# Performance work log

Hardware: AMD Instinct MI355X
Metric: run time of the kernel (lower is better)

The kernel has to match this reference:

```python
import jax, jax.numpy as jnp
import numpy as np

EPS = 1.0  # global `epsilon` in the original code
B, C, N, T = 4, 32, 256, 288
NUM_PRED, NUM_LOCAL = 12, 12
PERIOD, SHORT, LONG = 24, 12, 48
EMB = 16
RE_K = 5  # ResidualExtrapolate kernel width (num_input)


def const_extrap(x, p):
    # replicate-pad right by p along time
    return jnp.concatenate([x, jnp.repeat(x[..., -1:], p, axis=-1)], axis=-1)


def seasonal_extrap(x, p):
    # circular-pad right by p along time (p <= t)
    return jnp.concatenate([x, x[..., :p]], axis=-1)


def term_norm(x, L):
    # sliding-window mean/var over last axis, window L, replicate-padded left.
    pad1 = [(0, 0)] * 3 + [(1, 0)]
    cs = jnp.pad(jnp.cumsum(x, axis=-1), pad1)
    cs2 = jnp.pad(jnp.cumsum(x * x, axis=-1), pad1)
    mean = (cs[..., L:] - cs[..., :-L]) / L            # (b,c,n,t-L+1)
    var = (cs2[..., L:] - cs2[..., :-L]) / L - mean ** 2 + 1e-5
    padL = [(0, 0)] * 3 + [(L - 1, 0)]
    mean = jnp.pad(mean, padL, mode='edge')
    var = jnp.pad(var, padL, mode='edge')
    out = (x - mean) / jnp.sqrt(var + EPS)
    return out, mean, jnp.sqrt(var)


def seasonal_norm(x, P):
    b, c, n, t = x.shape
    xp = x.reshape(b, c, n, t // P, P)
    mean = xp.mean(3)                                   # (b,c,n,P) per-phase
    var = (xp ** 2).mean(3) - mean ** 2 + 1e-5
    mean = jnp.tile(mean, (1, 1, 1, t // P))
    var = jnp.tile(var, (1, 1, 1, t // P))
    out = (x - mean) / jnp.sqrt(var + EPS)
    return out, mean, jnp.sqrt(var)


def spatial_norm(x, emb):
    n = emb.shape[0]
    adj = emb @ emb.T - 10.0 * jnp.eye(n, dtype=x.dtype)
    adj = jax.nn.softmax(adj, axis=-1)                  # (n,n)
    mean = jnp.einsum('nm,bcmt->bcnt', adj, x)
    var = jnp.einsum('nm,bcmt->bcnt', adj, x * x) - mean ** 2 + 1e-5
    out = (x - mean) / jnp.sqrt(var + EPS)
    return out, mean, jnp.sqrt(var)


def residual_extrap(x, W, bias):
    # Conv2d(c -> c*num_pred, kernel (1, RE_K)) on last RE_K steps, then cat.
    b, c, n, t = x.shape
    y = jnp.einsum('ock,bcnk->bon', W[:, :, 0, :], x[..., -RE_K:]) + bias[None, :, None]
    proj = y.reshape(b, NUM_PRED, c, n).transpose(0, 2, 3, 1)  # (b,c,n,num_pred)
    return jnp.concatenate([x, proj], axis=-1)


def conv_time(x, W, bias):
    y = jax.lax.conv_general_dilated(x, W, (1, 1), 'VALID',
                                     dimension_numbers=('NCHW', 'OIHW', 'NCHW'))
    return y + bias[None, :, None, None]


def conv1x1(x, W, bias):
    return jnp.einsum('oc,bcnt->bont', W[:, :, 0, 0], x) + bias[None, :, None, None]


def setup_inputs() -> dict:
    key = jax.random.key(0)
    ks = jax.random.split(key, 16)
    f32 = jnp.float32

    def w(k, shape, fan_in):
        return jax.random.normal(k, shape, dtype=f32) / np.sqrt(fan_in)

    inp = {
        'x': jax.random.normal(ks[0], (B, C, N, T), dtype=f32),
        'node_embedding': 0.1 * jax.random.normal(ks[1], (N, EMB), dtype=f32),
        'conv1_w': w(ks[6], (C, 13 * C, 1, NUM_LOCAL), 13 * C * NUM_LOCAL),
        'conv1_b': jnp.zeros((C,), f32),
        'conv2_w': w(ks[7], (C, 13 * C, 1, NUM_LOCAL), 13 * C * NUM_LOCAL),
        'conv2_b': jnp.zeros((C,), f32),
        'skip_w': w(ks[8], (C, C, 1, 1), C),
        'skip_b': jnp.zeros((C,), f32),
        'res_w': w(ks[9], (C, C, 1, 1), C),
        'res_b': jnp.zeros((C,), f32),
    }
    for i in range(4):
        inp[f're{i + 1}_w'] = w(ks[2 + i], (C * NUM_PRED, C, 1, RE_K), C * RE_K)
        inp[f're{i + 1}_b'] = jnp.zeros((C * NUM_PRED,), f32)
    return inp


def reference(x, node_embedding, conv1_w, conv1_b, conv2_w, conv2_b,
              skip_w, skip_b, res_w, res_b,
              re1_w, re1_b, re2_w, re2_b, re3_w, re3_b, re4_w, re4_b):
    xs, aux = [], []

    x_proj = const_extrap(x, NUM_PRED)
    zeros = jnp.zeros_like(x_proj)
    xs.append(x_proj); aux.append(zeros)

    x1, lt_mean, lt_std = term_norm(x, LONG)
    xp = residual_extrap(x1, re1_w, re1_b)
    mp, sp = const_extrap(lt_mean, NUM_PRED), const_extrap(lt_std, NUM_PRED)
    xs += [xp, mp, sp]; aux += [zeros, mp, sp]

    x2, se_mean, se_std = seasonal_norm(x1, PERIOD)
    xp = residual_extrap(x2, re2_w, re2_b)
    mp, sp = seasonal_extrap(se_mean, NUM_PRED), seasonal_extrap(se_std, NUM_PRED)
    xs += [xp, mp, sp]; aux += [zeros, mp, sp]

    x3, st_mean, st_std = term_norm(x2, SHORT)
    xp = residual_extrap(x3, re3_w, re3_b)
    mp, sp = const_extrap(st_mean, NUM_PRED), const_extrap(st_std, NUM_PRED)
    xs += [xp, mp, sp]; aux += [zeros, mp, sp]

    x4, sn_mean, sn_std = spatial_norm(x3, node_embedding)
    xp = residual_extrap(x4, re4_w, re4_b)
    mp, sp = const_extrap(sn_mean, NUM_PRED), const_extrap(sn_std, NUM_PRED)
    xs += [xp, mp, sp]; aux += [zeros, mp, sp]

    pad1 = [(0, 0)] * 3 + [(1, 0)]
    x_cat = jnp.pad(jnp.concatenate(xs, axis=1), pad1)      # (b,13c,n,T+P+1)
    a_cat = jnp.pad(jnp.concatenate(aux, axis=1), pad1)

    g1 = conv_time(x_cat, conv1_w, conv1_b)
    g2 = conv_time(x_cat, conv2_w, conv2_b)
    a1 = conv_time(a_cat, conv1_w, conv1_b)
    a2 = conv_time(a_cat, conv2_w, conv2_b)

    prod = g1 * g2
    x_z = conv1x1(prod[..., :-NUM_PRED], res_w, res_b)
    s = conv1x1(prod[..., -NUM_PRED:], skip_w, skip_b)
    s_aux = conv1x1((a1 * a2)[..., -NUM_PRED:], skip_w, skip_b)
    return (x_z, s_aux, s)
```

## Files before the change

### kernel.cpp

```cpp
#include <hip/hip_runtime.h>

typedef unsigned short u16;
typedef __attribute__((ext_vector_type(8))) short short8v;
typedef __attribute__((ext_vector_type(4))) float f32x4;

#define PSTR 304L
#define OFF_SAUX 9109504L
#define OFF_S    9502720L
#define CHSTR (32L*256L*PSTR)

static __device__ __forceinline__ float bf2f(u16 u) {
  return __uint_as_float(((unsigned int)u) << 16);
}
static __device__ __forceinline__ u16 f2bf(float f) {
  unsigned int i = __float_as_uint(f);
  i += 0x7FFFu + ((i >> 16) & 1u);
  return (u16)(i >> 16);
}

static __device__ __forceinline__ void gload16(const void* g, void* l) {
  __builtin_amdgcn_global_load_lds(
      (const __attribute__((address_space(1))) unsigned int*)g,
      (__attribute__((address_space(3))) unsigned int*)l, 16, 0, 0);
}

static __device__ void adj_body(int row, const float* __restrict__ emb,
                                u16* __restrict__ adjb) {
  const int m = threadIdx.x;
  __shared__ float sred[8];
  float er[16];
#pragma unroll
  for (int e = 0; e < 16; ++e) er[e] = emb[row * 16 + e];
  float d = 0.f;
#pragma unroll
  for (int e = 0; e < 16; ++e) d += er[e] * emb[m * 16 + e];
  if (m == row) d -= 10.f;
  float v = d;
#pragma unroll
  for (int off = 32; off; off >>= 1) v = fmaxf(v, __shfl_xor(v, off, 64));
  const int wid = m >> 6, lane = m & 63;
  if (lane == 0) sred[wid] = v;
  __syncthreads();
  const float mx = fmaxf(fmaxf(sred[0], sred[1]), fmaxf(sred[2], sred[3]));
  const float p = expf(d - mx);
  v = p;
#pragma unroll
  for (int off = 32; off; off >>= 1) v += __shfl_xor(v, off, 64);
  if (lane == 0) sred[4 + wid] = v;
  __syncthreads();
  const float sum = sred[4] + sred[5] + sred[6] + sred[7];
  adjb[row * 256 + m] = f2bf(p / sum);
}

static __device__ void prepw_body(int bid, const float* __restrict__ c1w,
                                  const float* __restrict__ c2w,
                                  u16* __restrict__ wB) {
  const int idx = bid * 256 + threadIdx.x;
  const int kk = idx >> 11;
  const int rem = idx & 2047;
  const int j = rem >> 5, chp = rem & 31;
  const int pslot = chp >> 3, chlo = chp & 7;
  const int sl = pslot ^ ((j >> 1) & 3);
  const int ch = sl * 8 + chlo;
  const int g = kk / 12, k = kk - g * 12;
  const int cin = g * 32 + ch;
  const float* src = (j < 32) ? c1w : c2w;
  const int jj = j & 31;
  wB[idx] = f2bf(src[(jj * 416 + cin) * 12 + k]);
}

static __device__ __forceinline__ void wscan2(float& s1, float& s2, int lane) {
#pragma unroll
  for (int off = 1; off < 64; off <<= 1) {
    float a = __shfl_up(s1, off, 64);
    float b = __shfl_up(s2, off, 64);
    if (lane >= off) { s1 += a; s2 += b; }
  }
}

static __device__ void norm_body(int bid, const float* __restrict__ x,
                                 u16* __restrict__ xcat) {
  const int wid = threadIdx.x >> 6, lane = threadIdx.x & 63;
  const long row = (long)bid * 4 + wid;
  const int b = (int)(row >> 13);
  const int c = (int)((row >> 8) & 31);
  const int n = (int)(row & 255);
  const float* xr = x + row * 288;
  __shared__ float bufA[4][304], bufB[4][304], cs1[4][312], cs2[4][312], sst[4][80];
  float* bA = bufA[wid];
  float* bB = bufB[wid];
  float* p1 = cs1[wid];
  float* p2 = cs2[wid];
  float* psm = sst[wid];
  float* psi = sst[wid] + 24;
  float* psd = sst[wid] + 48;
  const long chb = (long)b * 416 * 256 + n;

  for (int j = 0; j < 5; ++j) { int t = j * 64 + lane; if (t < 288) bA[t] = xr[t]; }

  auto scanbuf = [&](float* src) {
    float ca = 0.f, cb = 0.f;
    if (lane == 0) { p1[0] = 0.f; p2[0] = 0.f; }
    for (int j = 0; j < 5; ++j) {
      int t = j * 64 + lane;
      float v = (t < 288) ? src[t] : 0.f;
      float s1 = v, s2 = v * v;
      wscan2(s1, s2, lane);
      if (t < 288) { p1[t + 1] = ca + s1; p2[t + 1] = cb + s2; }
      ca += __shfl(s1, 63, 64);
      cb += __shfl(s2, 63, 64);
    }
  };

  scanbuf(bA);
  for (int j = 0; j < 5; ++j) {
    int t = j * 64 + lane; if (t >= 288) continue;
    float S, Q;
    if (t >= 47) { S = p1[t + 1] - p1[t - 47]; Q = p2[t + 1] - p2[t - 47]; }
    else         { S = p1[48];                 Q = p2[48]; }
    float m = S * (1.f / 48.f);
    float var = Q * (1.f / 48.f) - m * m + 1e-5f;
    float sd = sqrtf(var);
    float iv = rsqrtf(var + 1.f);
    float xv = bA[t];
    float x1 = (xv - m) * iv;
    bB[t] = x1;
    xcat[(chb + (long)(c)      * 256) * PSTR + 1 + t] = f2bf(xv);
    xcat[(chb + (long)(32 + c) * 256) * PSTR + 1 + t] = f2bf(x1);
    xcat[(chb + (long)(64 + c) * 256) * PSTR + 1 + t] = f2bf(m);
    xcat[(chb + (long)(96 + c) * 256) * PSTR + 1 + t] = f2bf(sd);
  }
  {
    float S = p1[288] - p1[240], Q = p2[288] - p2[240];
    float m = S * (1.f / 48.f);
    float var = Q * (1.f / 48.f) - m * m + 1e-5f;
    float sd = sqrtf(var);
    if (lane < 12) {
      xcat[(chb + (long)(c)      * 256) * PSTR + 289 + lane] = f2bf(bA[287]);
      xcat[(chb + (long)(64 + c) * 256) * PSTR + 289 + lane] = f2bf(m);
      xcat[(chb + (long)(96 + c) * 256) * PSTR + 289 + lane] = f2bf(sd);
    }
    if (lane == 0) {
      xcat[(chb + (long)(c)      * 256) * PSTR] = 0;
      xcat[(chb + (long)(32 + c) * 256) * PSTR] = 0;
      xcat[(chb + (long)(64 + c) * 256) * PSTR] = 0;
      xcat[(chb + (long)(96 + c) * 256) * PSTR] = 0;
    }
  }
  if (lane < 24) {
    float S = 0.f, Q = 0.f;
#pragma unroll
    for (int i2 = 0; i2 < 12; ++i2) { float v = bB[lane + 24 * i2]; S += v; Q += v * v; }
    float m = S * (1.f / 12.f);
    float var = Q * (1.f / 12.f) - m * m + 1e-5f;
    psm[lane] = m; psi[lane] = rsqrtf(var + 1.f); psd[lane] = sqrtf(var);
  }
  for (int j = 0; j < 5; ++j) {
    int t = j * 64 + lane; if (t >= 288) continue;
    int ph = t % 24;
    float m = psm[ph];
    float x2v = (bB[t] - m) * psi[ph];
    bA[t] = x2v;
    xcat[(chb + (long)(128 + c) * 256) * PSTR + 1 + t] = f2bf(x2v);
    xcat[(chb + (long)(160 + c) * 256) * PSTR + 1 + t] = f2bf(m);
    xcat[(chb + (long)(192 + c) * 256) * PSTR + 1 + t] = f2bf(psd[ph]);
  }
  if (lane < 12) {
    xcat[(chb + (long)(160 + c) * 256) * PSTR + 289 + lane] = f2bf(psm[lane]);
    xcat[(chb + (long)(192 + c) * 256) * PSTR + 289 + lane] = f2bf(psd[lane]);
  }
  if (lane == 0) {
    xcat[(chb + (long)(128 + c) * 256) * PSTR] = 0;
    xcat[(chb + (long)(160 + c) * 256) * PSTR] = 0;
    xcat[(chb + (long)(192 + c) * 256) * PSTR] = 0;
  }
  scanbuf(bA);
  for (int j = 0; j < 5; ++j) {
    int t = j * 64 + lane; if (t >= 288) continue;
    float S, Q;
    if (t >= 11) { S = p1[t + 1] - p1[t - 11]; Q = p2[t + 1] - p2[t - 11]; }
    else         { S = p1[12];                 Q = p2[12]; }
    float m = S * (1.f / 12.f);
    float var = Q * (1.f / 12.f) - m * m + 1e-5f;
    float sd = sqrtf(var);
    float iv = rsqrtf(var + 1.f);
    float x3v = (bA[t] - m) * iv;
    xcat[(chb + (long)(224 + c) * 256) * PSTR + 1 + t] = f2bf(x3v);
    xcat[(chb + (long)(256 + c) * 256) * PSTR + 1 + t] = f2bf(m);
    xcat[(chb + (long)(288 + c) * 256) * PSTR + 1 + t] = f2bf(sd);
  }
  {
    float S = p1[288] - p1[276], Q = p2[288] - p2[276];
    float m = S * (1.f / 12.f);
    float var = Q * (1.f / 12.f) - m * m + 1e-5f;
    float sd = sqrtf(var);
    if (lane < 12) {
      xcat[(chb + (long)(256 + c) * 256) * PSTR + 289 + lane] = f2bf(m);
      xcat[(chb + (long)(288 + c) * 256) * PSTR + 289 + lane] = f2bf(sd);
    }
    if (lane == 0) {
      xcat[(chb + (long)(224 + c) * 256) * PSTR] = 0;
      xcat[(chb + (long)(256 + c) * 256) * PSTR] = 0;
      xcat[(chb + (long)(288 + c) * 256) * PSTR] = 0;
    }
  }
}

__global__ __launch_bounds__(256) void k_front(const float* __restrict__ x,
    const float* __restrict__ emb, const float* __restrict__ c1w,
    const float* __restrict__ c2w, u16* __restrict__ xcat,
    u16* __restrict__ adjb, u16* __restrict__ wB) {
  const int bid = blockIdx.x;
  if (bid < 8192)       norm_body(bid, x, xcat);
  else if (bid < 8448)  adj_body(bid - 8192, emb, adjb);
  else                  prepw_body(bid - 8448, c1w, c2w, wB);
}

static __device__ void re_body(long gid, u16* __restrict__ xcat,
                               const float* __restrict__ W,
                               const float* __restrict__ bias, int srcch) {
  const int o = (int)(gid % 384);
  const long bn = gid / 384;
  const int n = (int)(bn & 255);
  const int b = (int)(bn >> 8);
  const float* wr = W + o * 160;
  float acc = bias[o];
  for (int c = 0; c < 32; ++c) {
    const long rb = ((long)(b * 416 + srcch + c) * 256 + n) * PSTR + 284;
#pragma unroll
    for (int k = 0; k < 5; ++k) acc += wr[c * 5 + k] * bf2f(xcat[rb + k]);
  }
  const int cd = o & 31, p = o >> 5;
  xcat[((long)(b * 416 + srcch + cd) * 256 + n) * PSTR + 289 + p] = f2bf(acc);
}

__global__ __launch_bounds__(256) void k_re4(u16* __restrict__ xcat,
                                             const float* __restrict__ W,
                                             const float* __restrict__ bias) {
  re_body((long)blockIdx.x * 256 + threadIdx.x, xcat, W, bias, 320);
}

static __device__ void spatial_body(int sid, u16* __restrict__ xcat,
                                    const u16* __restrict__ adjb) {
  const int gx = sid % 20;
  const int slice = sid / 20;
  const int tcn = gx >> 2, ncb = gx & 3;
  const int b = slice >> 5, c = slice & 31;
  const int t0 = tcn * 64, n0 = ncb * 64;
  const int tid = threadIdx.x;
  const int wid = tid >> 6, lane = tid & 63;
  const int wm = wid >> 1, wn = wid & 1;
  const int l15 = lane & 15, lq = lane >> 4;
  __shared__ __align__(16) u16 BT[2][64 * 40];
  __shared__ __align__(16) u16 BT2[2][64 * 40];
  const f32x4 vz = {0.f, 0.f, 0.f, 0.f};
  f32x4 aM[2][2], aV[2][2];
#pragma unroll
  for (int i = 0; i < 2; ++i)
#pragma unroll
    for (int j = 0; j < 2; ++j) { aM[i][j] = vz; aV[i][j] = vz; }
  const long base7 = (long)(b * 416 + 224 + c) * 256;
  u16 rv[8];
#pragma unroll
  for (int r = 0; r < 8; ++r) {
    int idx = tid + r * 256; int ml = idx >> 6, s = idx & 63;
    rv[r] = xcat[(base7 + ml) * PSTR + 1 + t0 + s];
  }
#pragma unroll
  for (int r = 0; r < 8; ++r) {
    int idx = tid + r * 256; int ml = idx >> 6, s = idx & 63;
    float v = bf2f(rv[r]);
    BT[0][s * 40 + ml] = rv[r];
    BT2[0][s * 40 + ml] = f2bf(v * v);
  }
  __syncthreads();
  int cur = 0;
  for (int kk = 0; kk < 8; ++kk) {
    u16 rn[8];
    if (kk < 7) {
#pragma unroll
      for (int r = 0; r < 8; ++r) {
        int idx = tid + r * 256; int ml = idx >> 6, s = idx & 63;
        rn[r] = xcat[(base7 + (long)((kk + 1) * 32 + ml)) * PSTR + 1 + t0 + s];
      }
    }
    const short8v a0 = *(const short8v*)(adjb + (long)(n0 + wm * 32 + l15) * 256 + kk * 32 + lq * 8);
    const short8v a1 = *(const short8v*)(adjb + (long)(n0 + wm * 32 + 16 + l15) * 256 + kk * 32 + lq * 8);
    const u16* bt = BT[cur];
    const u16* bq = BT2[cur];
    const short8v b0 = *(const short8v*)(bt + (wn * 32 + l15) * 40 + lq * 8);
    const short8v b1 = *(const short8v*)(bt + (wn * 32 + 16 + l15) * 40 + lq * 8);
    const short8v q0 = *(const short8v*)(bq + (wn * 32 + l15) * 40 + lq * 8);
    const short8v q1 = *(const short8v*)(bq + (wn * 32 + 16 + l15) * 40 + lq * 8);
    aM[0][0] = __builtin_amdgcn_mfma_f32_16x16x32_bf16(a0, b0, aM[0][0], 0, 0, 0);
    aM[0][1] = __builtin_amdgcn_mfma_f32_16x16x32_bf16(a0, b1, aM[0][1], 0, 0, 0);
    aM[1][0] = __builtin_amdgcn_mfma_f32_16x16x32_bf16(a1, b0, aM[1][0], 0, 0, 0);
    aM[1][1] = __builtin_amdgcn_mfma_f32_16x16x32_bf16(a1, b1, aM[1][1], 0, 0, 0);
    aV[0][0] = __builtin_amdgcn_mfma_f32_16x16x32_bf16(a0, q0, aV[0][0], 0, 0, 0);
    aV[0][1] = __builtin_amdgcn_mfma_f32_16x16x32_bf16(a0, q1, aV[0][1], 0, 0, 0);
    aV[1][0] = __builtin_amdgcn_mfma_f32_16x16x32_bf16(a1, q0, aV[1][0], 0, 0, 0);
    aV[1][1] = __builtin_amdgcn_mfma_f32_16x16x32_bf16(a1, q1, aV[1][1], 0, 0, 0);
    __syncthreads();
    if (kk < 7) {
#pragma unroll
      for (int r = 0; r < 8; ++r) {
        int idx = tid + r * 256; int ml = idx >> 6, s = idx & 63;
        float v = bf2f(rn[r]);
        BT[cur ^ 1][s * 40 + ml] = rn[r];
        BT2[cur ^ 1][s * 40 + ml] = f2bf(v * v);
      }
    }
    __syncthreads();
    cur ^= 1;
  }
#pragma unroll
  for (int mf = 0; mf < 2; ++mf)
#pragma unroll
    for (int nf = 0; nf < 2; ++nf)
#pragma unroll
      for (int e = 0; e < 4; ++e) {
        const int i = wm * 32 + mf * 16 + lq * 4 + e;
        const int j = wn * 32 + nf * 16 + l15;
        const int nn = n0 + i, tt2 = t0 + j;
        if (tt2 < 288) {
          const float mean = aM[mf][nf][e], ex2 = aV[mf][nf][e];
          const float var = ex2 - mean * mean + 1e-5f;
          const float sd = sqrtf(var);
          const float iv = rsqrtf(var + 1.f);
          const float x3c = bf2f(xcat[(base7 + nn) * PSTR + 1 + tt2]);
          const float x4 = (x3c - mean) * iv;
          const long r10 = ((long)(b * 416 + 320 + c) * 256 + nn) * PSTR;
          const long r11 = ((long)(b * 416 + 352 + c) * 256 + nn) * PSTR;
          const long r12 = ((long)(b * 416 + 384 + c) * 256 + nn) * PSTR;
          xcat[r10 + 1 + tt2] = f2bf(x4);
          xcat[r11 + 1 + tt2] = f2bf(mean);
          xcat[r12 + 1 + tt2] = f2bf(sd);
          if (tt2 == 287) {
            for (int p = 0; p < 12; ++p) {
              xcat[r11 + 289 + p] = f2bf(mean);
              xcat[r12 + 289 + p] = f2bf(sd);
            }
          }
          if (tt2 == 0) { xcat[r10] = 0; xcat[r11] = 0; xcat[r12] = 0; }
        }
      }
}

__global__ __launch_bounds__(256) void k_mid(u16* __restrict__ xcat,
    const u16* __restrict__ adjb,
    const float* __restrict__ w1, const float* __restrict__ b1,
    const float* __restrict__ w2, const float* __restrict__ b2,
    const float* __restrict__ w3, const float* __restrict__ b3) {
  const int bid = blockIdx.x;
  if (bid < 2560) { spatial_body(bid, xcat, adjb); return; }
  const int sub = bid - 2560;
  const int which = sub / 1536;
  const long gid = (long)(sub - which * 1536) * 256 + threadIdx.x;
  if (which == 0)      re_body(gid, xcat, w1, b1, 32);
  else if (which == 1) re_body(gid, xcat, w2, b2, 128);
  else                 re_body(gid, xcat, w3, b3, 224);
}

__global__ __launch_bounds__(256, 3) void k_convG(
    const u16* __restrict__ xcat, const u16* __restrict__ wB,
    const float* __restrict__ c1b, const float* __restrict__ c2b,
    const float* __restrict__ rsw, const float* __restrict__ rsb,
    const float* __restrict__ skw, const float* __restrict__ skb,
    float* __restrict__ out) {
  const int tc = blockIdx.x;
  const int by = blockIdx.y;
  const int b = by >> 6;
  const int tid = threadIdx.x;
  const int wid = tid >> 6, lane = tid & 63;
  const int n_abs = (by & 63) * 4 + wid;
  const int t0 = tc * 64;
  const int l15 = lane & 15, lq = lane >> 4;

  __shared__ __align__(16) unsigned char smem[41984];
  u16* Asm = (u16*)smem;
  u16* Bsm = (u16*)(smem + 25600);

  int sch[5], stk[5];
  const u16* baseR[5];
#pragma unroll
  for (int r = 0; r < 5; ++r) {
    int cc = r * 64 + lane;
    int s = cc / 10;
    int tk = cc - s * 10;
    sch[r] = s; stk[r] = tk;
    baseR[r] = xcat + ((long)(b * 416 + s) * 256 + n_abs) * PSTR + t0 + tk * 8;
  }
  u16* aw = Asm + wid * 3200;

#define AWRITE() { \
    _Pragma("unroll") \
    for (int r = 0; r < 5; ++r) { \
      u16 pc[8]; *(uint4*)pc = aR[r]; \
      const int pcol = ((((sch[r] >> 3) ^ stk[r]) & 3) << 3) + (sch[r] & 7); \
      _Pragma("unroll") \
      for (int e = 0; e < 8; ++e) aw[(stk[r] * 8 + e) * 40 + pcol] = pc[e]; \
    } }

  uint4 aR[5];
#pragma unroll
  for (int r = 0; r < 5; ++r) aR[r] = *(const uint4*)baseR[r];
  AWRITE();
#pragma unroll
  for (int r = 0; r < 5; ++r) aR[r] = *(const uint4*)(baseR[r] + CHSTR);
  gload16(wB + 0 * 2048 + wid * 512 + lane * 8, Bsm + 0 + wid * 512);
  gload16(wB + 1 * 2048 + wid * 512 + lane * 8, Bsm + 2048 + wid * 512);
  __syncthreads();

  const f32x4 vz = {0.f, 0.f, 0.f, 0.f};
  f32x4 acc[4][4];
#pragma unroll
  for (int i = 0; i < 4; ++i)
#pragma unroll
    for (int j = 0; j < 4; ++j) acc[i][j] = vz;

  const u16* bwl = Bsm + l15 * 32 + ((lq ^ ((l15 >> 1) & 3)) << 3);

  int p = 0;
  for (int g = 0; g < 13; ++g) {
    for (int kp = 0; kp < 6; ++kp) {
      if (p < 77) {
        const long kkn = (long)(p + 1) * 2;
        const int bufn = ((p + 1) & 1) * 4096;
        gload16(wB + kkn * 2048 + wid * 512 + lane * 8, Bsm + bufn + wid * 512);
        gload16(wB + (kkn + 1) * 2048 + wid * 512 + lane * 8, Bsm + bufn + 2048 + wid * 512);
      }
      const int bufc = (p & 1) * 4096;
#pragma unroll
      for (int kh = 0; kh < 2; ++kh) {
        const int K = kp * 2 + kh;
        short8v af[4], bf[4];
#pragma unroll
        for (int f = 0; f < 4; ++f) {
          const int tt = K + f * 16 + l15;
          af[f] = *(const short8v*)(aw + tt * 40 + (((lq ^ (tt >> 3)) & 3) << 3));
        }
#pragma unroll
        for (int f = 0; f < 4; ++f)
          bf[f] = *(const short8v*)(bwl + bufc + kh * 2048 + f * 512);
#pragma unroll
        for (int i = 0; i < 4; ++i)
#pragma unroll
          for (int j = 0; j < 4; ++j)
            acc[i][j] = __builtin_amdgcn_mfma_f32_16x16x32_bf16(af[i], bf[j], acc[i][j], 0, 0, 0);
      }
      __syncthreads();
      ++p;
    }
    if (g < 12) {
      AWRITE();
      if (g < 11) {
#pragma unroll
        for (int r = 0; r < 5; ++r) aR[r] = *(const uint4*)(baseR[r] + (long)(g + 2) * CHSTR);
      }
    }
  }
#undef AWRITE
  __syncthreads();

  float* pw = (float*)smem + wid * 2112;
#pragma unroll
  for (int fi = 0; fi < 4; ++fi)
#pragma unroll
    for (int nf = 0; nf < 2; ++nf)
#pragma unroll
      for (int e = 0; e < 4; ++e) {
        const int trow = fi * 16 + lq * 4 + e;
        const int cch = nf * 16 + l15;
        const float g1 = acc[fi][nf][e] + c1b[cch];
        const float g2 = acc[fi][nf + 2][e] + c2b[cch];
        pw[trow * 33 + cch] = g1 * g2;
      }
  float pv[32];
  {
    const float* prow = pw + lane * 33;
#pragma unroll
    for (int c = 0; c < 32; ++c) pv[c] = prow[c];
  }
  const int t = t0 + lane;
  if (t0 + 63 < 278) {
    for (int o = 0; o < 32; ++o) {
      float s = rsb[o];
      const float* wr = rsw + o * 32;
#pragma unroll
      for (int c = 0; c < 32; ++c) s += wr[c] * pv[c];
      out[((long)(b * 32 + o) * 256 + n_abs) * 278 + t] = s;
    }
  } else {
    const bool isres = t < 278;
    const bool isskip = (t >= 278) && (t < 290);
    for (int o = 0; o < 32; ++o) {
      const float* wr = (isres ? rsw : skw) + o * 32;
      float s = (isres ? rsb : skb)[o];
#pragma unroll
      for (int c = 0; c < 32; ++c) s += wr[c] * pv[c];
      if (isres)       out[((long)(b * 32 + o) * 256 + n_abs) * 278 + t] = s;
      else if (isskip) out[OFF_S + ((long)(b * 32 + o) * 256 + n_abs) * 12 + (t - 278)] = s;
    }
  }
}

__global__ __launch_bounds__(256) void k_convA(const u16* __restrict__ xcat,
    const u16* __restrict__ wB, const float* __restrict__ c1b,
    const float* __restrict__ c2b, const float* __restrict__ skw,
    const float* __restrict__ skb, float* __restrict__ out) {
  const int tid = threadIdx.x;
  const int wid = tid >> 6, lane = tid & 63;
  const int row = blockIdx.x;
  const int b = row >> 8, n = row & 255;
  const int l15 = lane & 15, lq = lane >> 4;
  __shared__ __align__(16) u16 ATa[4][2][36 * 40];
  __shared__ float apL[4][16 * 68];
  const int gtab[8] = {2, 3, 5, 6, 8, 9, 11, 12};
  const long bnbase = (long)b * 416 * 256 + n;

#pragma unroll
  for (int tau = 0; tau < 2; ++tau) {
    const int g = gtab[wid * 2 + tau];
    u16* at = ATa[wid][tau];
#pragma unroll
    for (int h = 0; h < 2; ++h) {
      const int c = lane + h * 64;
      const int ch = c >> 2, part = c & 3;
      const uint4 v = *(const uint4*)(xcat +
          (bnbase + (long)(g * 32 + ch) * 256) * PSTR + 272 + part * 8);
      u16 pc[8]; *(uint4*)pc = v;
#pragma unroll
      for (int e = 0; e < 8; ++e) at[(part * 8 + e) * 40 + ch] = pc[e];
    }
  }

  const f32x4 vz = {0.f, 0.f, 0.f, 0.f};
  f32x4 acc[4] = {vz, vz, vz, vz};
  const int bsw = (lq ^ ((l15 >> 1) & 3)) << 3;
#pragma unroll
  for (int tau = 0; tau < 2; ++tau) {
    const int g = gtab[wid * 2 + tau];
    const u16* at = ATa[wid][tau];
    for (int k = 0; k < 12; ++k) {
      const short8v af = *(const short8v*)(at + (l15 + k + 6) * 40 + lq * 8);
#pragma unroll
      for (int nf = 0; nf < 4; ++nf) {
        const short8v bf = *(const short8v*)(wB + (long)(g * 12 + k) * 2048 + (nf * 16 + l15) * 32 + bsw);
        acc[nf] = __builtin_amdgcn_mfma_f32_16x16x32_bf16(af, bf, acc[nf], 0, 0, 0);
      }
    }
  }
  float* ap = apL[wid];
#pragma unroll
  for (int nf = 0; nf < 4; ++nf)
#pragma unroll
    for (int e = 0; e < 4; ++e)
      ap[(lq * 4 + e) * 68 + nf * 16 + l15] = acc[nf][e];
  __syncthreads();
  for (int idx = tid; idx < 1024; idx += 256) {
    const int m = idx >> 6, j = idx & 63;
    apL[0][m * 68 + j] = apL[0][m * 68 + j] + apL[1][m * 68 + j]
                       + apL[2][m * 68 + j] + apL[3][m * 68 + j];
  }
  __syncthreads();
  for (int task = tid; task < 384; task += 256) {
    const int o = task & 31, tt = task >> 5;
    float s = skb[o];
#pragma unroll
    for (int c2 = 0; c2 < 32; ++c2)
      s += skw[o * 32 + c2] * (apL[0][tt * 68 + c2] + c1b[c2])
                            * (apL[0][tt * 68 + 32 + c2] + c2b[c2]);
    out[OFF_SAUX + ((long)(b * 32 + o) * 256 + n) * 12 + tt] = s;
  }
}

extern "C" void kernel_launch(void* const* d_in, const int* in_sizes, int n_in,
                              void* d_out, int out_size, void* d_ws, size_t ws_size,
                              hipStream_t stream) {
  const float* x   = (const float*)d_in[0];
  const float* emb = (const float*)d_in[1];
  const float* c1w = (const float*)d_in[2];
  const float* c1b = (const float*)d_in[3];
  const float* c2w = (const float*)d_in[4];
  const float* c2b = (const float*)d_in[5];
  const float* skw = (const float*)d_in[6];
  const float* skb = (const float*)d_in[7];
  const float* rsw = (const float*)d_in[8];
  const float* rsb = (const float*)d_in[9];
  float* out = (float*)d_out;

  u16* xcat = (u16*)d_ws;
  u16* wB   = xcat + (4L * 416 * 256 * 304 + 2048);
  u16* adjb = wB + 156L * 2048;

  k_front<<<dim3(9696), dim3(256), 0, stream>>>(x, emb, c1w, c2w, xcat, adjb, wB);
  k_mid<<<dim3(7168), dim3(256), 0, stream>>>(xcat, adjb,
      (const float*)d_in[10], (const float*)d_in[11],
      (const float*)d_in[12], (const float*)d_in[13],
      (const float*)d_in[14], (const float*)d_in[15]);
  k_re4<<<dim3(1536), dim3(256), 0, stream>>>(xcat, (const float*)d_in[16], (const float*)d_in[17]);
  k_convG<<<dim3(5, 256), dim3(256), 0, stream>>>(xcat, wB, c1b, c2b, rsw, rsb, skw, skb, out);
  k_convA<<<dim3(1024), dim3(256), 0, stream>>>(xcat, wB, c1b, c2b, skw, skb, out);
}
```

Measured before the change: 676.7 us.

## Widen convG time tile to 128 so each weight tile feeds more MFMAs

The gated conv kernel now has a templated body. The first two time-chunks of each row handle 128 time steps per block (8 M-fragments), and the last chunk keeps 64, so the grid drops from 5 to 3 blocks in x. The goal is to reuse every B (weight) tile loaded into LDS over twice as many MFMAs and to cut the count of redundant weight streams. In exchange the kernel uses more accumulator registers and more LDS (62 KB), occupancy falls to 2 blocks per CU, and the blocks are unevenly loaded.

```diff
diff --git a/kernel.cpp b/kernel.cpp
--- a/kernel.cpp
+++ b/kernel.cpp
@@ -361,60 +361,58 @@
   else                 re_body(gid, xcat, w3, b3, 224);
 }
 
-__global__ __launch_bounds__(256, 3) void k_convG(
+template<int MT>
+static __device__ void convG_body(int t0, int by,
     const u16* __restrict__ xcat, const u16* __restrict__ wB,
     const float* __restrict__ c1b, const float* __restrict__ c2b,
     const float* __restrict__ rsw, const float* __restrict__ rsb,
     const float* __restrict__ skw, const float* __restrict__ skb,
-    float* __restrict__ out) {
-  const int tc = blockIdx.x;
-  const int by = blockIdx.y;
+    float* __restrict__ out, unsigned char* smem) {
   const int b = by >> 6;
   const int tid = threadIdx.x;
   const int wid = tid >> 6, lane = tid & 63;
   const int n_abs = (by & 63) * 4 + wid;
-  const int t0 = tc * 64;
   const int l15 = lane & 15, lq = lane >> 4;
-
-  __shared__ __align__(16) unsigned char smem[41984];
+  constexpr int NCH = (MT == 2) ? 9 : 5;
+  constexpr int TKS = (MT == 2) ? 18 : 10;
+
   u16* Asm = (u16*)smem;
-  u16* Bsm = (u16*)(smem + 25600);
-
-  int sch[5], stk[5];
-  const u16* baseR[5];
-#pragma unroll
-  for (int r = 0; r < 5; ++r) {
+  u16* Bsm = (u16*)(smem + 46080);
+
+  int sch[NCH], stk[NCH];
+  const u16* baseR[NCH];
+#pragma unroll
+  for (int r = 0; r < NCH; ++r) {
     int cc = r * 64 + lane;
-    int s = cc / 10;
-    int tk = cc - s * 10;
+    int s = cc / TKS, tk = cc - s * TKS;
     sch[r] = s; stk[r] = tk;
     baseR[r] = xcat + ((long)(b * 416 + s) * 256 + n_abs) * PSTR + t0 + tk * 8;
   }
-  u16* aw = Asm + wid * 3200;
+  u16* aw = Asm + wid * 5760;
 
 #define AWRITE() { \
     _Pragma("unroll") \
-    for (int r = 0; r < 5; ++r) { \
+    for (int r = 0; r < NCH; ++r) { \
       u16 pc[8]; *(uint4*)pc = aR[r]; \
       const int pcol = ((((sch[r] >> 3) ^ stk[r]) & 3) << 3) + (sch[r] & 7); \
       _Pragma("unroll") \
       for (int e = 0; e < 8; ++e) aw[(stk[r] * 8 + e) * 40 + pcol] = pc[e]; \
     } }
 
-  uint4 aR[5];
-#pragma unroll
-  for (int r = 0; r < 5; ++r) aR[r] = *(const uint4*)baseR[r];
+  uint4 aR[NCH];
+#pragma unroll
+  for (int r = 0; r < NCH; ++r) aR[r] = *(const uint4*)baseR[r];
   AWRITE();
 #pragma unroll
-  for (int r = 0; r < 5; ++r) aR[r] = *(const uint4*)(baseR[r] + CHSTR);
+  for (int r = 0; r < NCH; ++r) aR[r] = *(const uint4*)(baseR[r] + CHSTR);
   gload16(wB + 0 * 2048 + wid * 512 + lane * 8, Bsm + 0 + wid * 512);
   gload16(wB + 1 * 2048 + wid * 512 + lane * 8, Bsm + 2048 + wid * 512);
   __syncthreads();
 
   const f32x4 vz = {0.f, 0.f, 0.f, 0.f};
-  f32x4 acc[4][4];
-#pragma unroll
-  for (int i = 0; i < 4; ++i)
+  f32x4 acc[4 * MT][4];
+#pragma unroll
+  for (int i = 0; i < 4 * MT; ++i)
 #pragma unroll
     for (int j = 0; j < 4; ++j) acc[i][j] = vz;
 
@@ -433,9 +431,9 @@
 #pragma unroll
       for (int kh = 0; kh < 2; ++kh) {
         const int K = kp * 2 + kh;
-        short8v af[4], bf[4];
-#pragma unroll
-        for (int f = 0; f < 4; ++f) {
+        short8v af[4 * MT], bf[4];
+#pragma unroll
+        for (int f = 0; f < 4 * MT; ++f) {
           const int tt = K + f * 16 + l15;
           af[f] = *(const short8v*)(aw + tt * 40 + (((lq ^ (tt >> 3)) & 3) << 3));
         }
@@ -443,7 +441,7 @@
         for (int f = 0; f < 4; ++f)
           bf[f] = *(const short8v*)(bwl + bufc + kh * 2048 + f * 512);
 #pragma unroll
-        for (int i = 0; i < 4; ++i)
+        for (int i = 0; i < 4 * MT; ++i)
 #pragma unroll
           for (int j = 0; j < 4; ++j)
             acc[i][j] = __builtin_amdgcn_mfma_f32_16x16x32_bf16(af[i], bf[j], acc[i][j], 0, 0, 0);
@@ -455,53 +453,69 @@
       AWRITE();
       if (g < 11) {
 #pragma unroll
-        for (int r = 0; r < 5; ++r) aR[r] = *(const uint4*)(baseR[r] + (long)(g + 2) * CHSTR);
+        for (int r = 0; r < NCH; ++r) aR[r] = *(const uint4*)(baseR[r] + (long)(g + 2) * CHSTR);
       }
     }
   }
 #undef AWRITE
   __syncthreads();
 
-  float* pw = (float*)smem + wid * 2112;
-#pragma unroll
-  for (int fi = 0; fi < 4; ++fi)
-#pragma unroll
-    for (int nf = 0; nf < 2; ++nf)
-#pragma unroll
-      for (int e = 0; e < 4; ++e) {
-        const int trow = fi * 16 + lq * 4 + e;
-        const int cch = nf * 16 + l15;
-        const float g1 = acc[fi][nf][e] + c1b[cch];
-        const float g2 = acc[fi][nf + 2][e] + c2b[cch];
-        pw[trow * 33 + cch] = g1 * g2;
-      }
-  float pv[32];
-  {
-    const float* prow = pw + lane * 33;
-#pragma unroll
-    for (int c = 0; c < 32; ++c) pv[c] = prow[c];
-  }
-  const int t = t0 + lane;
-  if (t0 + 63 < 278) {
-    for (int o = 0; o < 32; ++o) {
-      float s = rsb[o];
-      const float* wr = rsw + o * 32;
-#pragma unroll
-      for (int c = 0; c < 32; ++c) s += wr[c] * pv[c];
-      out[((long)(b * 32 + o) * 256 + n_abs) * 278 + t] = s;
-    }
-  } else {
-    const bool isres = t < 278;
-    const bool isskip = (t >= 278) && (t < 290);
-    for (int o = 0; o < 32; ++o) {
-      const float* wr = (isres ? rsw : skw) + o * 32;
-      float s = (isres ? rsb : skb)[o];
-#pragma unroll
-      for (int c = 0; c < 32; ++c) s += wr[c] * pv[c];
-      if (isres)       out[((long)(b * 32 + o) * 256 + n_abs) * 278 + t] = s;
-      else if (isskip) out[OFF_S + ((long)(b * 32 + o) * 256 + n_abs) * 12 + (t - 278)] = s;
-    }
-  }
+#pragma unroll
+  for (int pass = 0; pass < MT; ++pass) {
+    float* pw = (float*)smem + wid * 2112;
+#pragma unroll
+    for (int fi = 0; fi < 4; ++fi)
+#pragma unroll
+      for (int nf = 0; nf < 2; ++nf)
+#pragma unroll
+        for (int e = 0; e < 4; ++e) {
+          const int trow = fi * 16 + lq * 4 + e;
+          const int cch = nf * 16 + l15;
+          const float g1 = acc[pass * 4 + fi][nf][e] + c1b[cch];
+          const float g2 = acc[pass * 4 + fi][nf + 2][e] + c2b[cch];
+          pw[trow * 33 + cch] = g1 * g2;
+        }
+    float pv[32];
+    {
+      const float* prow = pw + lane * 33;
+#pragma unroll
+      for (int c = 0; c < 32; ++c) pv[c] = prow[c];
+    }
+    const int t = t0 + pass * 64 + lane;
+    if (t0 + pass * 64 + 63 < 278) {
+      for (int o = 0; o < 32; ++o) {
+        float s = rsb[o];
+        const float* wr = rsw + o * 32;
+#pragma unroll
+        for (int c = 0; c < 32; ++c) s += wr[c] * pv[c];
+        out[((long)(b * 32 + o) * 256 + n_abs) * 278 + t] = s;
+      }
+    } else {
+      const bool isres = t < 278;
+      const bool isskip = (t >= 278) && (t < 290);
+      for (int o = 0; o < 32; ++o) {
+        const float* wr = (isres ? rsw : skw) + o * 32;
+        float s = (isres ? rsb : skb)[o];
+#pragma unroll
+        for (int c = 0; c < 32; ++c) s += wr[c] * pv[c];
+        if (isres)       out[((long)(b * 32 + o) * 256 + n_abs) * 278 + t] = s;
+        else if (isskip) out[OFF_S + ((long)(b * 32 + o) * 256 + n_abs) * 12 + (t - 278)] = s;
+      }
+    }
+  }
+}
+
+__global__ __launch_bounds__(256, 2) void k_convG(
+    const u16* __restrict__ xcat, const u16* __restrict__ wB,
+    const float* __restrict__ c1b, const float* __restrict__ c2b,
+    const float* __restrict__ rsw, const float* __restrict__ rsb,
+    const float* __restrict__ skw, const float* __restrict__ skb,
+    float* __restrict__ out) {
+  __shared__ __align__(16) unsigned char smem[62464];
+  if (blockIdx.x < 2)
+    convG_body<2>(blockIdx.x * 128, blockIdx.y, xcat, wB, c1b, c2b, rsw, rsb, skw, skb, out, smem);
+  else
+    convG_body<1>(256, blockIdx.y, xcat, wB, c1b, c2b, rsw, rsb, skw, skb, out, smem);
 }
 
 __global__ __launch_bounds__(256) void k_convA(const u16* __restrict__ xcat,
@@ -599,6 +613,6 @@
       (const float*)d_in[12], (const float*)d_in[13],
       (const float*)d_in[14], (const float*)d_in[15]);
   k_re4<<<dim3(1536), dim3(256), 0, stream>>>(xcat, (const float*)d_in[16], (const float*)d_in[17]);
-  k_convG<<<dim3(5, 256), dim3(256), 0, stream>>>(xcat, wB, c1b, c2b, rsw, rsb, skw, skb, out);
+  k_convG<<<dim3(3, 256), dim3(256), 0, stream>>>(xcat, wB, c1b, c2b, rsw, rsb, skw, skb, out);
   k_convA<<<dim3(1024), dim3(256), 0, stream>>>(xcat, wB, c1b, c2b, skw, skb, out);
 }
```

After: 604.9 us, median of 3. -10.6%, faster.
